# Kernel tuning notes

Hardware: AMD Instinct MI355X
Metric: run time of the kernel (lower is better)

The kernel has to match this reference:

```python
import jax, jax.numpy as jnp
import numpy as np

B, S, D, H = 4, 2048, 1024, 16
DK = D // H  # 64


def setup_inputs() -> dict:
    key = jax.random.key(0)
    ks = jax.random.split(key, 5)
    scale = 1.0 / np.sqrt(D)
    return {
        "embeddings": jax.random.normal(ks[0], (B, S, D), dtype=jnp.float32),
        "W_q": jax.random.normal(ks[1], (D, D), dtype=jnp.float32) * scale,
        "W_k": jax.random.normal(ks[2], (D, D), dtype=jnp.float32) * scale,
        "W_v": jax.random.normal(ks[3], (D, D), dtype=jnp.float32) * scale,
        "W_o": jax.random.normal(ks[4], (D, D), dtype=jnp.float32) * scale,
    }


def reference(embeddings, W_q, W_k, W_v, W_o):
    # torch nn.Linear: y = x @ W.T  (weights are [out, in])
    b, s, d = embeddings.shape
    h, dk = H, DK
    q = embeddings @ W_q.T  # [b, s, d]
    k = embeddings @ W_k.T
    v = embeddings @ W_v.T
    # split heads along last dim (matches the per-head slicing in the torch loop)
    q = q.reshape(b, s, h, dk)
    k = k.reshape(b, s, h, dk)
    v = v.reshape(b, s, h, dk)
    scores = jnp.einsum("bqhd,bkhd->bhqk", q, k) / jnp.sqrt(jnp.float32(dk))
    p = jax.nn.softmax(scores, axis=-1)  # dropout is identity at eval
    ctx = jnp.einsum("bhqk,bkhd->bqhd", p, v).reshape(b, s, d)
    return ctx @ W_o.T
```

## Files before the change

kernel.cpp:

```cpp
#include <hip/hip_runtime.h>
#include <hip/hip_bf16.h>

typedef unsigned short u16;
typedef __attribute__((ext_vector_type(8))) short bf16x8;
typedef __attribute__((ext_vector_type(4))) float f32x4;

#define AS1 __attribute__((address_space(1)))
#define AS3 __attribute__((address_space(3)))

constexpr int Bc = 4, Sc = 2048, Dc = 1024, Hc = 16, DKc = 64;
constexpr size_t EDc = (size_t)Bc * Sc * Dc;
constexpr size_t WDc = (size_t)Dc * Dc;

__device__ __forceinline__ void g2l16(const void* g, void* l) {
  __builtin_amdgcn_global_load_lds((const AS1 unsigned int*)g,
                                   (AS3 unsigned int*)l, 16, 0, 0);
}

__device__ __forceinline__ u16 f2b(float f) {
  union { float f; unsigned u; } x; x.f = f;
  unsigned r = x.u + 0x7fffu + ((x.u >> 16) & 1u);
  return (u16)(r >> 16);
}

__global__ __launch_bounds__(256)
void cvt_all(const float* __restrict__ e, const float* __restrict__ wq,
             const float* __restrict__ wk, const float* __restrict__ wv,
             const float* __restrict__ wo, u16* __restrict__ dst) {
  int bx = blockIdx.x;
  const float* src;
  size_t doff;
  int chunk;
  if (bx < 4096) {
    src = e; doff = 0; chunk = bx;
  } else {
    int t = bx - 4096;
    int w = t >> 9;
    chunk = t & 511;
    src = (w == 0) ? wq : (w == 1) ? wk : (w == 2) ? wv : wo;
    doff = EDc + (size_t)w * WDc;
  }
  size_t i = ((size_t)chunk * 256 + threadIdx.x) * 8;
  float4 a = *(const float4*)(src + i);
  float4 b = *(const float4*)(src + i + 4);
  bf16x8 o;
  o[0] = (short)f2b(a.x); o[1] = (short)f2b(a.y);
  o[2] = (short)f2b(a.z); o[3] = (short)f2b(a.w);
  o[4] = (short)f2b(b.x); o[5] = (short)f2b(b.y);
  o[6] = (short)f2b(b.z); o[7] = (short)f2b(b.w);
  *(bf16x8*)(dst + doff + i) = o;
}

__global__ __launch_bounds__(256, 2)
void gemm_qkv(const u16* __restrict__ X, const u16* __restrict__ Wq,
              const u16* __restrict__ Wk, const u16* __restrict__ Wv,
              u16* __restrict__ Qo, u16* __restrict__ Ko,
              u16* __restrict__ VTo) {
  constexpr int BM = 128, BK = 64, K = Dc, N = Dc;
  __shared__ u16 As[BM * BK];
  __shared__ u16 Bs[BM * BK];

  const int tid = threadIdx.x;
  const int wave = tid >> 6, lane = tid & 63;
  const int mr = lane & 15, quad = lane >> 4, mr7 = lane & 7;
  const int sect = blockIdx.x >> 3;
  const int n0 = (blockIdx.x & 7) * 128;
  const int m0 = blockIdx.y * BM;
  const u16* W = (sect == 0) ? Wq : (sect == 1) ? Wk : Wv;
  const int wm = (wave >> 1) * 64, wn = (wave & 1) * 64;
  const int ldr = lane >> 3;
  const int ldc_sw = ((lane & 7) ^ (ldr & 7)) * 8;

  const f32x4 zero = {0.f, 0.f, 0.f, 0.f};
  f32x4 acc[4][4];
  #pragma unroll
  for (int i = 0; i < 4; i++)
    #pragma unroll
    for (int j = 0; j < 4; j++) acc[i][j] = zero;

  for (int k0 = 0; k0 < K; k0 += BK) {
    __syncthreads();
    #pragma unroll
    for (int i = 0; i < 4; i++) {
      int row = wave * 32 + i * 8;
      g2l16(X + (size_t)(m0 + row + ldr) * K + k0 + ldc_sw, As + row * BK);
      g2l16(W + (size_t)(n0 + row + ldr) * K + k0 + ldc_sw, Bs + row * BK);
    }
    __syncthreads();

    #pragma unroll
    for (int c = 0; c < 2; c++) {
      bf16x8 a[4], b[4];
      #pragma unroll
      for (int i = 0; i < 4; i++)
        a[i] = *(const bf16x8*)(As + (wm + i * 16 + mr) * BK +
                                (((c * 4 + quad) ^ mr7) * 8));
      #pragma unroll
      for (int j = 0; j < 4; j++)
        b[j] = *(const bf16x8*)(Bs + (wn + j * 16 + mr) * BK +
                                (((c * 4 + quad) ^ mr7) * 8));
      #pragma unroll
      for (int i = 0; i < 4; i++)
        #pragma unroll
        for (int j = 0; j < 4; j++)
          acc[i][j] = __builtin_amdgcn_mfma_f32_16x16x32_bf16(
              a[i], b[j], acc[i][j], 0, 0, 0);
    }
  }

  if (sect == 2) {
    #pragma unroll
    for (int i = 0; i < 4; i++)
      #pragma unroll
      for (int j = 0; j < 4; j++) {
        int mbase = m0 + wm + i * 16 + quad * 4;
        int n = n0 + wn + j * 16 + mr;
        int b = mbase >> 11, s = mbase & 2047;
        int h = n >> 6, d = n & 63;
        ushort4 pk;
        pk.x = f2b(acc[i][j][0]); pk.y = f2b(acc[i][j][1]);
        pk.z = f2b(acc[i][j][2]); pk.w = f2b(acc[i][j][3]);
        *(ushort4*)(VTo + ((size_t)((b * Hc + h) * DKc + d)) * Sc + s) = pk;
      }
  } else {
    const float scale = (sect == 0) ? 0.125f : 1.0f;
    u16* Y = (sect == 0) ? Qo : Ko;
    #pragma unroll
    for (int i = 0; i < 4; i++)
      #pragma unroll
      for (int j = 0; j < 4; j++)
        #pragma unroll
        for (int r = 0; r < 4; r++) {
          int m = m0 + wm + i * 16 + quad * 4 + r;
          int n = n0 + wn + j * 16 + mr;
          Y[(size_t)m * N + n] = f2b(acc[i][j][r] * scale);
        }
  }
}

__global__ __launch_bounds__(256, 2)
void gemm_out(const u16* __restrict__ X, const u16* __restrict__ W,
              float* __restrict__ Y, int M, int N, int K) {
  constexpr int BM = 128, BK = 64;
  __shared__ u16 As[BM * BK];
  __shared__ u16 Bs[BM * BK];

  const int tid = threadIdx.x;
  const int wave = tid >> 6, lane = tid & 63;
  const int mr = lane & 15, quad = lane >> 4, mr7 = lane & 7;
  const int m0 = blockIdx.y * BM, n0 = blockIdx.x * BM;
  const int wm = (wave >> 1) * 64, wn = (wave & 1) * 64;
  const int ldr = lane >> 3;
  const int ldc_sw = ((lane & 7) ^ (ldr & 7)) * 8;

  const f32x4 zero = {0.f, 0.f, 0.f, 0.f};
  f32x4 acc[4][4];
  #pragma unroll
  for (int i = 0; i < 4; i++)
    #pragma unroll
    for (int j = 0; j < 4; j++) acc[i][j] = zero;

  for (int k0 = 0; k0 < K; k0 += BK) {
    __syncthreads();
    #pragma unroll
    for (int i = 0; i < 4; i++) {
      int row = wave * 32 + i * 8;
      g2l16(X + (size_t)(m0 + row + ldr) * K + k0 + ldc_sw, As + row * BK);
      g2l16(W + (size_t)(n0 + row + ldr) * K + k0 + ldc_sw, Bs + row * BK);
    }
    __syncthreads();

    #pragma unroll
    for (int c = 0; c < 2; c++) {
      bf16x8 a[4], b[4];
      #pragma unroll
      for (int i = 0; i < 4; i++)
        a[i] = *(const bf16x8*)(As + (wm + i * 16 + mr) * BK +
                                (((c * 4 + quad) ^ mr7) * 8));
      #pragma unroll
      for (int j = 0; j < 4; j++)
        b[j] = *(const bf16x8*)(Bs + (wn + j * 16 + mr) * BK +
                                (((c * 4 + quad) ^ mr7) * 8));
      #pragma unroll
      for (int i = 0; i < 4; i++)
        #pragma unroll
        for (int j = 0; j < 4; j++)
          acc[i][j] = __builtin_amdgcn_mfma_f32_16x16x32_bf16(
              a[i], b[j], acc[i][j], 0, 0, 0);
    }
  }

  #pragma unroll
  for (int i = 0; i < 4; i++)
    #pragma unroll
    for (int j = 0; j < 4; j++)
      #pragma unroll
      for (int r = 0; r < 4; r++) {
        int m = m0 + wm + i * 16 + quad * 4 + r;
        int n = n0 + wn + j * 16 + mr;
        Y[(size_t)m * N + n] = acc[i][j][r];
      }
}

__device__ __forceinline__ void softmax_tile(f32x4* s, float* lR, u16* Pw,
                                             int quad, int mr, int mr7,
                                             bf16x8* pa) {
  #pragma unroll
  for (int r = 0; r < 4; r++) {
    int prow = quad * 4 + r, p7 = prow & 7;
    #pragma unroll
    for (int kc = 0; kc < 4; kc++) {
      float p = __expf(fminf(s[kc][r], 60.f));
      lR[r] += p;
      Pw[prow * 64 + (((kc * 2 + (mr >> 3)) ^ p7) * 8) + mr7] = f2b(p);
    }
  }
  #pragma unroll
  for (int c = 0; c < 2; c++)
    pa[c] = *(const bf16x8*)(Pw + mr * 64 + (((c * 4 + quad) ^ mr7) * 8));
}

__global__ __launch_bounds__(256, 3)
void attn(const u16* __restrict__ Q, const u16* __restrict__ K,
          const u16* __restrict__ VT, u16* __restrict__ O) {
  __shared__ u16 Ks[64 * 64];
  __shared__ u16 Vs[64 * 64];
  __shared__ u16 Ps[4][16 * 64];

  const int tid = threadIdx.x;
  const int wave = tid >> 6, lane = tid & 63;
  const int mr = lane & 15, quad = lane >> 4, mr7 = lane & 7;
  const int bh = blockIdx.y;
  const int b = bh >> 4, h = bh & 15;
  const int q0 = blockIdx.x * 128;
  const size_t headK = (size_t)b * Sc * Dc + (size_t)h * DKc;
  const size_t headV = (size_t)bh * DKc * Sc;
  const int ldr = lane >> 3;
  const int ldc_sw = ((lane & 7) ^ (ldr & 7)) * 8;

  bf16x8 qa[2][2];
  #pragma unroll
  for (int t = 0; t < 2; t++)
    #pragma unroll
    for (int c = 0; c < 2; c++)
      qa[t][c] = *(const bf16x8*)(Q + headK +
          (size_t)(q0 + wave * 32 + t * 16 + mr) * Dc + c * 32 + quad * 8);

  const f32x4 zero = {0.f, 0.f, 0.f, 0.f};
  f32x4 o[2][4];
  float lrow[2][4];
  #pragma unroll
  for (int t = 0; t < 2; t++)
    #pragma unroll
    for (int i = 0; i < 4; i++) {
      o[t][i] = zero;
      lrow[t][i] = 0.f;
    }

  for (int kt = 0; kt < Sc / 64; kt++) {
    const int k0 = kt * 64;
    __syncthreads();
    #pragma unroll
    for (int i = 0; i < 2; i++) {
      int row = wave * 16 + i * 8;
      g2l16(K + headK + (size_t)(k0 + row + ldr) * Dc + ldc_sw, Ks + row * 64);
      g2l16(VT + headV + (size_t)(row + ldr) * Sc + k0 + ldc_sw, Vs + row * 64);
    }
    __syncthreads();

    f32x4 s0[4], s1[4];
    #pragma unroll
    for (int kc = 0; kc < 4; kc++) {
      s0[kc] = zero; s1[kc] = zero;
      #pragma unroll
      for (int c = 0; c < 2; c++) {
        bf16x8 kb = *(const bf16x8*)(Ks + (kc * 16 + mr) * 64 +
                                     (((c * 4 + quad) ^ mr7) * 8));
        s0[kc] = __builtin_amdgcn_mfma_f32_16x16x32_bf16(qa[0][c], kb, s0[kc], 0, 0, 0);
        s1[kc] = __builtin_amdgcn_mfma_f32_16x16x32_bf16(qa[1][c], kb, s1[kc], 0, 0, 0);
      }
    }

    bf16x8 pa[2][2];
    softmax_tile(s0, lrow[0], Ps[wave], quad, mr, mr7, pa[0]);
    softmax_tile(s1, lrow[1], Ps[wave], quad, mr, mr7, pa[1]);

    #pragma unroll
    for (int ni = 0; ni < 4; ni++)
      #pragma unroll
      for (int c = 0; c < 2; c++) {
        bf16x8 vb = *(const bf16x8*)(Vs + (ni * 16 + mr) * 64 +
                                     (((c * 4 + quad) ^ mr7) * 8));
        o[0][ni] = __builtin_amdgcn_mfma_f32_16x16x32_bf16(pa[0][c], vb, o[0][ni], 0, 0, 0);
        o[1][ni] = __builtin_amdgcn_mfma_f32_16x16x32_bf16(pa[1][c], vb, o[1][ni], 0, 0, 0);
      }
  }

  #pragma unroll
  for (int t = 0; t < 2; t++)
    #pragma unroll
    for (int r = 0; r < 4; r++) {
      float l = lrow[t][r];
      #pragma unroll
      for (int off = 1; off < 16; off <<= 1)
        l += __shfl_xor(l, off, 64);
      float inv = 1.0f / l;
      #pragma unroll
      for (int ni = 0; ni < 4; ni++) {
        int qq = q0 + wave * 32 + t * 16 + quad * 4 + r;
        O[headK + (size_t)qq * Dc + ni * 16 + mr] = f2b(o[t][ni][r] * inv);
      }
    }
}

extern "C" void kernel_launch(void* const* d_in, const int* in_sizes, int n_in,
                              void* d_out, int out_size, void* d_ws, size_t ws_size,
                              hipStream_t stream) {
  const float* emb = (const float*)d_in[0];
  const float* Wq  = (const float*)d_in[1];
  const float* Wk  = (const float*)d_in[2];
  const float* Wv  = (const float*)d_in[3];
  const float* Wo  = (const float*)d_in[4];
  float* out = (float*)d_out;

  const int M = Bc * Sc;

  u16* Eb  = (u16*)d_ws;
  u16* Wqb = Eb  + EDc;
  u16* Wkb = Wqb + WDc;
  u16* Wvb = Wkb + WDc;
  u16* Wob = Wvb + WDc;
  u16* Qb  = Wob + WDc;
  u16* Kb  = Qb  + EDc;
  u16* VTb = Kb  + EDc;
  u16* Cb  = Qb;

  dim3 blk(256);
  cvt_all<<<dim3(4096 + 4 * 512), blk, 0, stream>>>(emb, Wq, Wk, Wv, Wo, Eb);

  gemm_qkv<<<dim3(24, M / 128), blk, 0, stream>>>(Eb, Wqb, Wkb, Wvb,
                                                  Qb, Kb, VTb);

  attn<<<dim3(Sc / 128, Bc * Hc), blk, 0, stream>>>(Qb, Kb, VTb, Cb);

  gemm_out<<<dim3(Dc / 128, M / 128), blk, 0, stream>>>(Cb, Wob, out,
                                                        M, Dc, Dc);
}
```

Baseline: 293.5 us.

## Permute K rows to pack P stores, use exp2 softmax and packed bf16 conversion

```diff
diff --git a/kernel.cpp b/kernel.cpp
--- a/kernel.cpp
+++ b/kernel.cpp
@@ -4,6 +4,7 @@
 typedef unsigned short u16;
 typedef __attribute__((ext_vector_type(8))) short bf16x8;
 typedef __attribute__((ext_vector_type(4))) float f32x4;
+typedef __attribute__((ext_vector_type(2))) unsigned int u32x2;
 
 #define AS1 __attribute__((address_space(1)))
 #define AS3 __attribute__((address_space(3)))
@@ -21,6 +22,27 @@
   union { float f; unsigned u; } x; x.f = f;
   unsigned r = x.u + 0x7fffu + ((x.u >> 16) & 1u);
   return (u16)(r >> 16);
+}
+
+#if __has_builtin(__builtin_amdgcn_cvt_pk_bf16_f32)
+typedef __attribute__((ext_vector_type(2))) __bf16 hbf2;
+__device__ __forceinline__ unsigned f2b_pk(float a, float b) {
+  union { hbf2 v; unsigned u; } x;
+  x.v = __builtin_amdgcn_cvt_pk_bf16_f32(a, b);
+  return x.u;
+}
+#else
+__device__ __forceinline__ unsigned f2b_pk(float a, float b) {
+  return (unsigned)f2b(a) | ((unsigned)f2b(b) << 16);
+}
+#endif
+
+__device__ __forceinline__ float fast_exp2(float x) {
+#if __has_builtin(__builtin_amdgcn_exp2f)
+  return __builtin_amdgcn_exp2f(x);
+#else
+  return exp2f(x);
+#endif
 }
 
 __global__ __launch_bounds__(256)
@@ -123,7 +145,7 @@
         *(ushort4*)(VTo + ((size_t)((b * Hc + h) * DKc + d)) * Sc + s) = pk;
       }
   } else {
-    const float scale = (sect == 0) ? 0.125f : 1.0f;
+    const float scale = (sect == 0) ? 0.18033688f : 1.0f;
     u16* Y = (sect == 0) ? Qo : Ko;
     #pragma unroll
     for (int i = 0; i < 4; i++)
@@ -202,25 +224,7 @@
       }
 }
 
-__device__ __forceinline__ void softmax_tile(f32x4* s, float* lR, u16* Pw,
-                                             int quad, int mr, int mr7,
-                                             bf16x8* pa) {
-  #pragma unroll
-  for (int r = 0; r < 4; r++) {
-    int prow = quad * 4 + r, p7 = prow & 7;
-    #pragma unroll
-    for (int kc = 0; kc < 4; kc++) {
-      float p = __expf(fminf(s[kc][r], 60.f));
-      lR[r] += p;
-      Pw[prow * 64 + (((kc * 2 + (mr >> 3)) ^ p7) * 8) + mr7] = f2b(p);
-    }
-  }
-  #pragma unroll
-  for (int c = 0; c < 2; c++)
-    pa[c] = *(const bf16x8*)(Pw + mr * 64 + (((c * 4 + quad) ^ mr7) * 8));
-}
-
-__global__ __launch_bounds__(256, 3)
+__global__ __launch_bounds__(256, 4)
 void attn(const u16* __restrict__ Q, const u16* __restrict__ K,
           const u16* __restrict__ VT, u16* __restrict__ O) {
   __shared__ u16 Ks[64 * 64];
@@ -257,14 +261,18 @@
       lrow[t][i] = 0.f;
     }
 
+  u16* Pw = Ps[wave];
+
   for (int kt = 0; kt < Sc / 64; kt++) {
     const int k0 = kt * 64;
     __syncthreads();
     #pragma unroll
     for (int i = 0; i < 2; i++) {
-      int row = wave * 16 + i * 8;
-      g2l16(K + headK + (size_t)(k0 + row + ldr) * Dc + ldc_sw, Ks + row * 64);
-      g2l16(VT + headV + (size_t)(row + ldr) * Sc + k0 + ldc_sw, Vs + row * 64);
+      int row0 = wave * 16 + i * 8;
+      int p = row0 + ldr;
+      int srow = ((p & 15) << 2) | (p >> 4);
+      g2l16(K + headK + (size_t)(k0 + srow) * Dc + ldc_sw, Ks + row0 * 64);
+      g2l16(VT + headV + (size_t)(row0 + ldr) * Sc + k0 + ldc_sw, Vs + row0 * 64);
     }
     __syncthreads();
 
@@ -282,8 +290,26 @@
     }
 
     bf16x8 pa[2][2];
-    softmax_tile(s0, lrow[0], Ps[wave], quad, mr, mr7, pa[0]);
-    softmax_tile(s1, lrow[1], Ps[wave], quad, mr, mr7, pa[1]);
+    #pragma unroll
+    for (int t = 0; t < 2; t++) {
+      f32x4* s = t ? s1 : s0;
+      float* lR = lrow[t];
+      #pragma unroll
+      for (int r = 0; r < 4; r++) {
+        float p0 = fast_exp2(fminf(s[0][r], 100.f));
+        float p1 = fast_exp2(fminf(s[1][r], 100.f));
+        float p2 = fast_exp2(fminf(s[2][r], 100.f));
+        float p3 = fast_exp2(fminf(s[3][r], 100.f));
+        lR[r] += (p0 + p1) + (p2 + p3);
+        u32x2 w;
+        w.x = f2b_pk(p0, p1);
+        w.y = f2b_pk(p2, p3);
+        *(u32x2*)(Pw + (quad * 4 + r) * 64 + mr * 4) = w;
+      }
+      #pragma unroll
+      for (int c = 0; c < 2; c++)
+        pa[t][c] = *(const bf16x8*)(Pw + mr * 64 + c * 32 + quad * 8);
+    }
 
     #pragma unroll
     for (int ni = 0; ni < 4; ni++)
```

Measured after the change: 299.1 us. No clear change (+1.9%).
